# Kernel optimization log

Hardware: AMD Instinct MI355X
Metric: run time of the kernel (lower is better)

## Reference

```python
import jax, jax.numpy as jnp
import numpy as np

HIDDEN = 1024

def setup_inputs() -> dict:
    key = jax.random.key(0)
    ks = jax.random.split(key, 8)
    B, Ti, Tt, V, H, U, K = 4, 2048, 2048, 32000, 1024, 4096, 3
    return {
        "inputs": jax.random.randint(ks[0], (B, Ti), 0, V, dtype=jnp.int32),
        "targets": jax.random.randint(ks[1], (B, Tt), 0, V, dtype=jnp.int32),
        "input_emb": jax.random.normal(ks[2], (V, H), jnp.float32) * 0.02,
        "target_emb": jax.random.normal(ks[3], (V, H), jnp.float32) * 0.02,
        "conv_w": jax.random.normal(ks[4], (K, H, U), jnp.float32) * 0.02,
        "conv_b": jnp.zeros((U,), jnp.float32),
        "dense_w": jax.random.normal(ks[5], (U, H), jnp.float32) * 0.02,
        "dense_b": jnp.zeros((H,), jnp.float32),
    }

def reference(inputs, targets, input_emb, target_emb, conv_w, conv_b, dense_w, dense_b):
    emb_scale = jnp.asarray(HIDDEN, jnp.float32) ** 0.5
    # EmbeddingSharedWeights: gather + sqrt(hidden) scaling
    ie = jnp.take(input_emb, inputs, axis=0) * emb_scale    # [B, Ti, H]
    te = jnp.take(target_emb, targets, axis=0) * emb_scale  # [B, Tt, H]
    # manual scaled dot-product cross-attention (no masks: defaults are None)
    dk = jnp.asarray(ie.shape[-1], jnp.float32)
    logits = jnp.einsum("btd,bsd->bts", te, ie) / jnp.sqrt(dk)  # [B, Tt, Ti]
    weights = jax.nn.softmax(logits, axis=-1)
    attn = jnp.einsum("bts,bsd->btd", weights, ie)              # [B, Tt, H]
    # LanguageModel: Conv1D(units, kernel_size, same) + relu + Dense(hidden)
    h = jax.lax.conv_general_dilated(
        attn, conv_w, window_strides=(1,), padding="SAME",
        dimension_numbers=("NWC", "WIO", "NWC")) + conv_b        # [B, Tt, U]
    h = jax.nn.relu(h)
    out = jnp.einsum("btu,uh->bth", h, dense_w) + dense_b       # [B, Tt, H]
    return out
```

## Files before the change

### kernel.cpp

```cpp
#include <hip/hip_runtime.h>
#include <cstddef>

static constexpr int HID = 1024;
static constexpr int NB  = 4;
static constexpr int TT  = 2048;
static constexpr int UD  = 4096;
static constexpr int PR  = TT + 1;

typedef short bf8    __attribute__((ext_vector_type(8)));
typedef float f32x4  __attribute__((ext_vector_type(4)));

__device__ __forceinline__ unsigned short f2bf(float x) {
  unsigned int u = __float_as_uint(x);
  u += 0x7fffu + ((u >> 16) & 1u);
  return (unsigned short)(u >> 16);
}
__device__ __forceinline__ float bf2f(unsigned short h) {
  return __uint_as_float(((unsigned int)h) << 16);
}
__device__ __forceinline__ unsigned short cvt_bf(float x) { return f2bf(x); }
__device__ __forceinline__ unsigned short cvt_bf(unsigned short x) { return x; }

__device__ __forceinline__ void g2l16(const unsigned short* g, unsigned short* l) {
  __builtin_amdgcn_global_load_lds(
      (const __attribute__((address_space(1))) unsigned int*)g,
      (__attribute__((address_space(3))) unsigned int*)l, 16, 0, 0);
}

#define BARX() __builtin_amdgcn_s_barrier()
#define VMCNT(n) asm volatile("s_waitcnt vmcnt(" #n ")" ::: "memory")

__device__ __forceinline__ void xcd_swz(int& bx, int& by, int& bz) {
  const int gx = gridDim.x, gy = gridDim.y;
  const int nwg = gx * gy * (int)gridDim.z;
  int flat = bx + gx * (by + gy * bz);
  const int cpx = nwg >> 3;
  flat = (flat & 7) * cpx + (flat >> 3);
  bx = flat % gx; flat /= gx;
  by = flat % gy; bz = flat / gy;
}

__global__ __launch_bounds__(256) void gather_split_k(
    const int* __restrict__ idx, const float* __restrict__ emb,
    unsigned short* __restrict__ hi, unsigned short* __restrict__ lo, float scale)
{
  const int row = blockIdx.x;
  const int r = idx[row];
  const int c = threadIdx.x * 4;
  float4 v = *(const float4*)(emb + (size_t)r * HID + c);
  v.x *= scale; v.y *= scale; v.z *= scale; v.w *= scale;
  ushort4 h, l;
  h.x = f2bf(v.x); h.y = f2bf(v.y); h.z = f2bf(v.z); h.w = f2bf(v.w);
  l.x = f2bf(v.x - bf2f(h.x)); l.y = f2bf(v.y - bf2f(h.y));
  l.z = f2bf(v.z - bf2f(h.z)); l.w = f2bf(v.w - bf2f(h.w));
  *(ushort4*)(hi + (size_t)row * HID + c) = h;
  *(ushort4*)(lo + (size_t)row * HID + c) = l;
}

__global__ __launch_bounds__(256) void zero_guard_k(unsigned short* __restrict__ p)
{
  unsigned short* row = p + (size_t)blockIdx.x * PR * HID;
  *(ushort4*)(row + threadIdx.x * 4) = (ushort4){0, 0, 0, 0};
}

template<typename TIN>
__global__ __launch_bounds__(256) void transpose_bf_k(
    const TIN* __restrict__ in, unsigned short* __restrict__ out,
    int R, int C, long long sIn, long long sOut)
{
  __shared__ unsigned short tile[32][33];
  in  += (size_t)blockIdx.z * sIn;
  out += (size_t)blockIdx.z * sOut;
  const int r0 = blockIdx.y * 32, c0 = blockIdx.x * 32;
  const int tc = threadIdx.x & 31, tr8 = threadIdx.x >> 5;
#pragma unroll
  for (int p = 0; p < 4; ++p) {
    const int r = tr8 + p * 8;
    tile[r][tc] = cvt_bf(in[(size_t)(r0 + r) * C + c0 + tc]);
  }
  __syncthreads();
#pragma unroll
  for (int p = 0; p < 4; ++p) {
    const int c = tr8 + p * 8;
    out[(size_t)(c0 + c) * R + r0 + tc] = tile[tc][c];
  }
}

__global__ __launch_bounds__(256) void softmax_bf_k(
    const float* __restrict__ L, unsigned short* __restrict__ W)
{
  const float* row = L + (size_t)blockIdx.x * TT;
  unsigned short* wout = W + (size_t)blockIdx.x * TT;
  const int tid = threadIdx.x;
  float4 v0 = ((const float4*)row)[tid * 2];
  float4 v1 = ((const float4*)row)[tid * 2 + 1];
  float mx = fmaxf(fmaxf(fmaxf(v0.x, v0.y), fmaxf(v0.z, v0.w)),
                   fmaxf(fmaxf(v1.x, v1.y), fmaxf(v1.z, v1.w)));
#pragma unroll
  for (int off = 32; off > 0; off >>= 1)
    mx = fmaxf(mx, __shfl_xor(mx, off, 64));
  __shared__ float sred[8];
  const int wid = tid >> 6;
  if ((tid & 63) == 0) sred[wid] = mx;
  __syncthreads();
  mx = fmaxf(fmaxf(sred[0], sred[1]), fmaxf(sred[2], sred[3]));
  v0.x = __expf(v0.x - mx); v0.y = __expf(v0.y - mx);
  v0.z = __expf(v0.z - mx); v0.w = __expf(v0.w - mx);
  v1.x = __expf(v1.x - mx); v1.y = __expf(v1.y - mx);
  v1.z = __expf(v1.z - mx); v1.w = __expf(v1.w - mx);
  float s = v0.x + v0.y + v0.z + v0.w + v1.x + v1.y + v1.z + v1.w;
#pragma unroll
  for (int off = 32; off > 0; off >>= 1)
    s += __shfl_xor(s, off, 64);
  if ((tid & 63) == 0) sred[4 + wid] = s;
  __syncthreads();
  s = sred[4] + sred[5] + sred[6] + sred[7];
  const float inv = 1.0f / s;
  ushort4 o0, o1;
  o0.x = f2bf(v0.x * inv); o0.y = f2bf(v0.y * inv);
  o0.z = f2bf(v0.z * inv); o0.w = f2bf(v0.w * inv);
  o1.x = f2bf(v1.x * inv); o1.y = f2bf(v1.y * inv);
  o1.z = f2bf(v1.z * inv); o1.w = f2bf(v1.w * inv);
  *(ushort4*)(wout + tid * 8)     = o0;
  *(ushort4*)(wout + tid * 8 + 4) = o1;
}

__device__ __forceinline__ void stage256(
    const unsigned short* __restrict__ P, int ld, int r0, int kk,
    unsigned short* lds, int tid)
{
  const int ke = (((tid & 3) ^ ((tid >> 3) & 3)) << 3);
  const int row = r0 + (tid >> 2);
  g2l16(P + (size_t)row * ld + kk + ke, lds + tid * 8);
  g2l16(P + (size_t)(row + 128) * ld + kk + ke, lds + 4096 + tid * 8);
}
__device__ __forceinline__ void stage128(
    const unsigned short* __restrict__ P, int ld, int r0, int kk,
    unsigned short* lds, int tid)
{
  const int ke = (((tid & 3) ^ ((tid >> 3) & 3)) << 3);
  const int row = r0 + (tid >> 2);
  g2l16(P + (size_t)row * ld + kk + ke, lds + tid * 8);
}

template<int CONVA>
__device__ __forceinline__ void stage_half(
    const unsigned short* __restrict__ P, int ld, int r0, int t, int ks,
    unsigned short* lds, int tid)
{
  const int bk = t * 64 + ks * 32;
  const int ke = (((tid & 3) ^ ((tid >> 3) & 3)) << 3);
  int rowbase, kcol;
  if constexpr (CONVA) {
    const int seg = bk >> 10;
    kcol = (bk & 1023) + ke;
    rowbase = r0 + (tid >> 2) + seg - 1;
  } else {
    kcol = bk + ke;
    rowbase = r0 + (tid >> 2);
  }
#pragma unroll
  for (int c = 0; c < 2; ++c)
    g2l16(P + (ptrdiff_t)(rowbase + c * 128) * ld + kcol,
          lds + c * 4096 + tid * 8);
}

template<int OUTBF, int EPI, int CONVA>
__global__ __launch_bounds__(512, 2) void gemm256_k(
    const unsigned short* __restrict__ A, long long sA, int lda,
    const unsigned short* __restrict__ B, long long sB, int ldb,
    void* __restrict__ Cv, long long sC, int ldc,
    int K, const float* __restrict__ bias)
{
  __shared__ __align__(16) unsigned short As[2][2][256 * 32];
  __shared__ __align__(16) unsigned short Bs[2][2][256 * 32];
  const int tid = threadIdx.x;
  int bxi = blockIdx.x, byi = blockIdx.y, bzi = blockIdx.z;
  xcd_swz(bxi, byi, bzi);
  A += (size_t)bzi * sA;
  B += (size_t)bzi * sB;
  const int bm = byi * 256;
  const int bn = bxi * 256;
  const int wave = tid >> 6, lane = tid & 63;
  const int wr = wave >> 2, wcn = wave & 3;
  const int q = lane >> 4, l16 = lane & 15;
  const int ksw = ((q ^ ((l16 >> 1) & 3)) << 3);
  const int abase = (wr * 128 + l16) * 32 + ksw;
  const int bbase = (wcn * 64 + l16) * 32 + ksw;

  f32x4 acc[8][4];
#pragma unroll
  for (int i = 0; i < 8; ++i)
#pragma unroll
    for (int j = 0; j < 4; ++j)
      acc[i][j] = (f32x4){0.f, 0.f, 0.f, 0.f};

  const int T = K >> 6;

  stage_half<CONVA>(A, lda, bm, 0, 0, &As[0][0][0], tid);
  stage_half<0>   (B, ldb, bn, 0, 0, &Bs[0][0][0], tid);
  stage_half<CONVA>(A, lda, bm, 0, 1, &As[0][1][0], tid);
  stage_half<0>   (B, ldb, bn, 0, 1, &Bs[0][1][0], tid);
  VMCNT(4);
  BARX();

  bf8 af[4], bfr[4];
  for (int t = 0; t < T; ++t) {
    const int buf = t & 1;
    unsigned short* An0 = &As[buf ^ 1][0][0];
    unsigned short* An1 = &As[buf ^ 1][1][0];
    unsigned short* Bn0 = &Bs[buf ^ 1][0][0];
    unsigned short* Bn1 = &Bs[buf ^ 1][1][0];
    const bool next = (t + 1 < T);

#pragma unroll
    for (int j = 0; j < 4; ++j) bfr[j] = *(const bf8*)&Bs[buf][0][bbase + j * 512];
#pragma unroll
    for (int m = 0; m < 4; ++m) af[m] = *(const bf8*)&As[buf][0][abase + m * 512];
    if (next) stage_half<CONVA>(A, lda, bm, t + 1, 0, An0, tid);
    BARX();
    __builtin_amdgcn_s_setprio(1);
#pragma unroll
    for (int m = 0; m < 4; ++m)
#pragma unroll
      for (int j = 0; j < 4; ++j)
        acc[m][j] = __builtin_amdgcn_mfma_f32_16x16x32_bf16(af[m], bfr[j], acc[m][j], 0, 0, 0);
    __builtin_amdgcn_s_setprio(0);
    BARX();

#pragma unroll
    for (int m = 0; m < 4; ++m) af[m] = *(const bf8*)&As[buf][0][abase + (4 + m) * 512];
    if (next) { stage_half<0>(B, ldb, bn, t + 1, 0, Bn0, tid); VMCNT(4); }
    else      { VMCNT(0); }
    BARX();
    __builtin_amdgcn_s_setprio(1);
#pragma unroll
    for (int m = 0; m < 4; ++m)
#pragma unroll
      for (int j = 0; j < 4; ++j)
        acc[4 + m][j] = __builtin_amdgcn_mfma_f32_16x16x32_bf16(af[m], bfr[j], acc[4 + m][j], 0, 0, 0);
    __builtin_amdgcn_s_setprio(0);
    BARX();

#pragma unroll
    for (int j = 0; j < 4; ++j) bfr[j] = *(const bf8*)&Bs[buf][1][bbase + j * 512];
#pragma unroll
    for (int m = 0; m < 4; ++m) af[m] = *(const bf8*)&As[buf][1][abase + m * 512];
    if (next) stage_half<CONVA>(A, lda, bm, t + 1, 1, An1, tid);
    BARX();
    __builtin_amdgcn_s_setprio(1);
#pragma unroll
    for (int m = 0; m < 4; ++m)
#pragma unroll
      for (int j = 0; j < 4; ++j)
        acc[m][j] = __builtin_amdgcn_mfma_f32_16x16x32_bf16(af[m], bfr[j], acc[m][j], 0, 0, 0);
    __builtin_amdgcn_s_setprio(0);
    BARX();

#pragma unroll
    for (int m = 0; m < 4; ++m) af[m] = *(const bf8*)&As[buf][1][abase + (4 + m) * 512];
    if (next) { stage_half<0>(B, ldb, bn, t + 1, 1, Bn1, tid); VMCNT(4); }
    BARX();
    __builtin_amdgcn_s_setprio(1);
#pragma unroll
    for (int m = 0; m < 4; ++m)
#pragma unroll
      for (int j = 0; j < 4; ++j)
        acc[4 + m][j] = __builtin_amdgcn_mfma_f32_16x16x32_bf16(af[m], bfr[j], acc[4 + m][j], 0, 0, 0);
    __builtin_amdgcn_s_setprio(0);
    BARX();
  }

  float* Cf          = (float*)Cv          + (size_t)bzi * sC;
  unsigned short* Cb = (unsigned short*)Cv + (size_t)bzi * sC;
#pragma unroll
  for (int j = 0; j < 4; ++j) {
    const int col = bn + wcn * 64 + j * 16 + l16;
    float bv = 0.f;
    if constexpr (EPI >= 1) bv = bias[col];
#pragma unroll
    for (int i = 0; i < 8; ++i) {
      const int row0 = bm + wr * 128 + i * 16 + q * 4;
#pragma unroll
      for (int r = 0; r < 4; ++r) {
        float v = acc[i][j][r];
        if constexpr (EPI >= 1) v += bv;
        if constexpr (EPI == 2) v = fmaxf(v, 0.f);
        if constexpr (OUTBF) Cb[(size_t)(row0 + r) * ldc + col] = f2bf(v);
        else                 Cf[(size_t)(row0 + r) * ldc + col] = v;
      }
    }
  }
}

template<int OUTBF, int EPI>
__global__ __launch_bounds__(512, 2) void gemm128_k(
    const unsigned short* __restrict__ A, long long sA, int lda,
    const unsigned short* __restrict__ B, long long sB, int ldb,
    void* __restrict__ Cv, long long sC, int ldc,
    int K, const float* __restrict__ bias)
{
  __shared__ __align__(16) unsigned short As[2][2][128 * 32];
  __shared__ __align__(16) unsigned short Bs[2][2][256 * 32];
  const int tid = threadIdx.x;
  int bxi = blockIdx.x, byi = blockIdx.y, bzi = blockIdx.z;
  xcd_swz(bxi, byi, bzi);
  A += (size_t)bzi * sA;
  B += (size_t)bzi * sB;
  const int bm = byi * 128;
  const int bn = bxi * 256;
  const int wave = tid >> 6, lane = tid & 63;
  const int wr = wave >> 2, wcn = wave & 3;
  const int q = lane >> 4, l16 = lane & 15;
  const int ksw = ((q ^ ((l16 >> 1) & 3)) << 3);
  const int abase = (wr * 64 + l16) * 32 + ksw;
  const int bbase = (wcn * 64 + l16) * 32 + ksw;

  f32x4 acc[4][4];
#pragma unroll
  for (int i = 0; i < 4; ++i)
#pragma unroll
    for (int j = 0; j < 4; ++j)
      acc[i][j] = (f32x4){0.f, 0.f, 0.f, 0.f};

  const int T = K >> 6;

  stage128(A, lda, bm, 0,  &As[0][0][0], tid);
  stage256(B, ldb, bn, 0,  &Bs[0][0][0], tid);
  stage128(A, lda, bm, 32, &As[0][1][0], tid);
  stage256(B, ldb, bn, 32, &Bs[0][1][0], tid);
  VMCNT(3);
  BARX();

  bf8 af[4], bfr[4];
  for (int t = 0; t < T; ++t) {
    const int buf = t & 1;
    const bool next = (t + 1 < T);
    const int kk = (t + 1) * 64;

#pragma unroll
    for (int j = 0; j < 4; ++j) bfr[j] = *(const bf8*)&Bs[buf][0][bbase + j * 512];
#pragma unroll
    for (int m = 0; m < 4; ++m) af[m] = *(const bf8*)&As[buf][0][abase + m * 512];
    if (next) {
      stage128(A, lda, bm, kk,      &As[buf ^ 1][0][0], tid);
      stage256(B, ldb, bn, kk,      &Bs[buf ^ 1][0][0], tid);
      VMCNT(3);
    } else { VMCNT(0); }
    BARX();
    __builtin_amdgcn_s_setprio(1);
#pragma unroll
    for (int m = 0; m < 4; ++m)
#pragma unroll
      for (int j = 0; j < 4; ++j)
        acc[m][j] = __builtin_amdgcn_mfma_f32_16x16x32_bf16(af[m], bfr[j], acc[m][j], 0, 0, 0);
    __builtin_amdgcn_s_setprio(0);
    BARX();

#pragma unroll
    for (int j = 0; j < 4; ++j) bfr[j] = *(const bf8*)&Bs[buf][1][bbase + j * 512];
#pragma unroll
    for (int m = 0; m < 4; ++m) af[m] = *(const bf8*)&As[buf][1][abase + m * 512];
    if (next) {
      stage128(A, lda, bm, kk + 32, &As[buf ^ 1][1][0], tid);
      stage256(B, ldb, bn, kk + 32, &Bs[buf ^ 1][1][0], tid);
      VMCNT(3);
    }
    BARX();
    __builtin_amdgcn_s_setprio(1);
#pragma unroll
    for (int m = 0; m < 4; ++m)
#pragma unroll
      for (int j = 0; j < 4; ++j)
        acc[m][j] = __builtin_amdgcn_mfma_f32_16x16x32_bf16(af[m], bfr[j], acc[m][j], 0, 0, 0);
    __builtin_amdgcn_s_setprio(0);
    BARX();
  }

  float* Cf          = (float*)Cv          + (size_t)bzi * sC;
  unsigned short* Cb = (unsigned short*)Cv + (size_t)bzi * sC;
#pragma unroll
  for (int j = 0; j < 4; ++j) {
    const int col = bn + wcn * 64 + j * 16 + l16;
    float bv = 0.f;
    if constexpr (EPI >= 1) bv = bias[col];
#pragma unroll
    for (int i = 0; i < 4; ++i) {
      const int row0 = bm + wr * 64 + i * 16 + q * 4;
#pragma unroll
      for (int r = 0; r < 4; ++r) {
        float v = acc[i][j][r];
        if constexpr (EPI >= 1) v += bv;
        if constexpr (EPI == 2) v = fmaxf(v, 0.f);
        if constexpr (OUTBF) Cb[(size_t)(row0 + r) * ldc + col] = f2bf(v);
        else                 Cf[(size_t)(row0 + r) * ldc + col] = v;
      }
    }
  }
}

__global__ __launch_bounds__(512, 2) void gemm_logits256_k(
    const unsigned short* __restrict__ Ah, const unsigned short* __restrict__ Al,
    const unsigned short* __restrict__ Bh, const unsigned short* __restrict__ Bl,
    float* __restrict__ C)
{
  __shared__ __align__(16) unsigned short AsH[2][256 * 32];
  __shared__ __align__(16) unsigned short AsL[2][256 * 32];
  __shared__ __align__(16) unsigned short BsH[2][256 * 32];
  __shared__ __align__(16) unsigned short BsL[2][256 * 32];
  const int tid = threadIdx.x;
  int bxi = blockIdx.x, byi = blockIdx.y, bzi = blockIdx.z;
  xcd_swz(bxi, byi, bzi);
  const long long SE = (long long)TT * HID;
  Ah += (size_t)bzi * SE; Al += (size_t)bzi * SE;
  Bh += (size_t)bzi * SE; Bl += (size_t)bzi * SE;
  C  += (size_t)bzi * TT * TT;
  const int bm = byi * 256;
  const int bn = bxi * 256;
  const int wave = tid >> 6, lane = tid & 63;
  const int wr = wave >> 2, wcn = wave & 3;
  const int q = lane >> 4, l16 = lane & 15;
  const int ksw = ((q ^ ((l16 >> 1) & 3)) << 3);
  const int abase = (wr * 128 + l16) * 32 + ksw;
  const int bbase = (wcn * 64 + l16) * 32 + ksw;

  f32x4 acc[8][4];
#pragma unroll
  for (int i = 0; i < 8; ++i)
#pragma unroll
    for (int j = 0; j < 4; ++j)
      acc[i][j] = (f32x4){0.f, 0.f, 0.f, 0.f};

  const int T = HID / 32;

  stage256(Ah, HID, bm, 0, &AsH[0][0], tid);
  stage256(Bh, HID, bn, 0, &BsH[0][0], tid);
  stage256(Al, HID, bm, 0, &AsL[0][0], tid);
  stage256(Bl, HID, bn, 0, &BsL[0][0], tid);
  VMCNT(4);
  BARX();

  bf8 bh[4], bl[4], a0[4], a1[4], a2[4], a3[4];
  for (int t = 0; t < T; ++t) {
    const int buf = t & 1;
    const bool next = (t + 1 < T);
    const int kk = (t + 1) * 32;

#pragma unroll
    for (int j = 0; j < 4; ++j) bh[j] = *(const bf8*)&BsH[buf][bbase + j * 512];
#pragma unroll
    for (int m = 0; m < 4; ++m) a0[m] = *(const bf8*)&AsH[buf][abase + m * 512];
    if (next) stage256(Ah, HID, bm, kk, &AsH[buf ^ 1][0], tid);
    BARX();
    __builtin_amdgcn_s_setprio(1);
#pragma unroll
    for (int m = 0; m < 4; ++m)
#pragma unroll
      for (int j = 0; j < 4; ++j)
        acc[m][j] = __builtin_amdgcn_mfma_f32_16x16x32_bf16(a0[m], bh[j], acc[m][j], 0, 0, 0);
    __builtin_amdgcn_s_setprio(0);
    BARX();

#pragma unroll
    for (int m = 0; m < 4; ++m) a1[m] = *(const bf8*)&AsH[buf][abase + (4 + m) * 512];
    if (next) { stage256(Bh, HID, bn, kk, &BsH[buf ^ 1][0], tid); VMCNT(4); }
    else      { VMCNT(0); }
    BARX();
    __builtin_amdgcn_s_setprio(1);
#pragma unroll
    for (int m = 0; m < 4; ++m)
#pragma unroll
      for (int j = 0; j < 4; ++j)
        acc[4 + m][j] = __builtin_amdgcn_mfma_f32_16x16x32_bf16(a1[m], bh[j], acc[4 + m][j], 0, 0, 0);
    __builtin_amdgcn_s_setprio(0);
    BARX();

#pragma unroll
    for (int j = 0; j < 4; ++j) bl[j] = *(const bf8*)&BsL[buf][bbase + j * 512];
#pragma unroll
    for (int m = 0; m < 4; ++m) a2[m] = *(const bf8*)&AsL[buf][abase + m * 512];
    if (next) stage256(Al, HID, bm, kk, &AsL[buf ^ 1][0], tid);
    BARX();
    __builtin_amdgcn_s_setprio(1);
#pragma unroll
    for (int m = 0; m < 4; ++m)
#pragma unroll
      for (int j = 0; j < 4; ++j) {
        acc[m][j] = __builtin_amdgcn_mfma_f32_16x16x32_bf16(a0[m], bl[j], acc[m][j], 0, 0, 0);
        acc[m][j] = __builtin_amdgcn_mfma_f32_16x16x32_bf16(a2[m], bh[j], acc[m][j], 0, 0, 0);
      }
    __builtin_amdgcn_s_setprio(0);
    BARX();

#pragma unroll
    for (int m = 0; m < 4; ++m) a3[m] = *(const bf8*)&AsL[buf][abase + (4 + m) * 512];
    if (next) { stage256(Bl, HID, bn, kk, &BsL[buf ^ 1][0], tid); VMCNT(4); }
    BARX();
    __builtin_amdgcn_s_setprio(1);
#pragma unroll
    for (int m = 0; m < 4; ++m)
#pragma unroll
      for (int j = 0; j < 4; ++j) {
        acc[4 + m][j] = __builtin_amdgcn_mfma_f32_16x16x32_bf16(a1[m], bl[j], acc[4 + m][j], 0, 0, 0);
        acc[4 + m][j] = __builtin_amdgcn_mfma_f32_16x16x32_bf16(a3[m], bh[j], acc[4 + m][j], 0, 0, 0);
      }
    __builtin_amdgcn_s_setprio(0);
    BARX();
  }

#pragma unroll
  for (int j = 0; j < 4; ++j) {
    const int col = bn + wcn * 64 + j * 16 + l16;
#pragma unroll
    for (int i = 0; i < 8; ++i) {
      const int row0 = bm + wr * 128 + i * 16 + q * 4;
#pragma unroll
      for (int r = 0; r < 4; ++r)
        C[(size_t)(row0 + r) * TT + col] = acc[i][j][r];
    }
  }
}

extern "C" void kernel_launch(void* const* d_in, const int* in_sizes, int n_in,
                              void* d_out, int out_size, void* d_ws, size_t ws_size,
                              hipStream_t stream)
{
  const int*   inputs     = (const int*)d_in[0];
  const int*   targets    = (const int*)d_in[1];
  const float* input_emb  = (const float*)d_in[2];
  const float* target_emb = (const float*)d_in[3];
  const float* conv_w     = (const float*)d_in[4];
  const float* conv_b     = (const float*)d_in[5];
  const float* dense_w    = (const float*)d_in[6];
  const float* dense_b    = (const float*)d_in[7];
  float* out = (float*)d_out;

  const long long SE = (long long)TT * HID;
  const size_t SZ = (size_t)NB * SE * 2;

  char* base = (char*)d_ws;
  unsigned short* te_hi = (unsigned short*)(base);
  unsigned short* te_lo = (unsigned short*)(base + SZ);
  unsigned short* ie_hi = (unsigned short*)(base + 2 * SZ);
  unsigned short* ie_lo = (unsigned short*)(base + 3 * SZ);
  float*          logit = (float*)         (base + 4 * SZ);
  unsigned short* Wbf   = (unsigned short*)(base + 4 * SZ + (size_t)NB * TT * TT * 4);
  unsigned short* ieT     = (unsigned short*)(base);
  unsigned short* attnP   = (unsigned short*)(base + SZ);
  unsigned short* attnD   = attnP + (size_t)HID;
  unsigned short* convwb  = (unsigned short*)(base + 2 * SZ + 16384);
  unsigned short* hb      = (unsigned short*)(base + 4 * SZ);
  unsigned short* densewb = (unsigned short*)Wbf;

  gather_split_k<<<NB * TT, 256, 0, stream>>>(targets, target_emb, te_hi, te_lo, 1.0f);
  gather_split_k<<<NB * TT, 256, 0, stream>>>(inputs,  input_emb,  ie_hi, ie_lo, 32.0f);

  gemm_logits256_k<<<dim3(TT / 256, TT / 256, NB), 512, 0, stream>>>(
      te_hi, te_lo, ie_hi, ie_lo, logit);

  transpose_bf_k<unsigned short><<<dim3(HID / 32, TT / 32, NB), 256, 0, stream>>>(
      ie_hi, ieT, TT, HID, SE, SE);

  softmax_bf_k<<<NB * TT, 256, 0, stream>>>(logit, Wbf);

  zero_guard_k<<<NB + 1, 256, 0, stream>>>(attnP);
  gemm128_k<1, 0><<<dim3(HID / 256, TT / 128, NB), 512, 0, stream>>>(
      Wbf, (long long)TT * TT, TT, ieT, SE, TT,
      attnD, (long long)PR * HID, HID, TT, nullptr);

  transpose_bf_k<float><<<dim3(UD / 32, (3 * HID) / 32, 1), 256, 0, stream>>>(
      conv_w, convwb, 3 * HID, UD, 0, 0);
  transpose_bf_k<float><<<dim3(HID / 32, UD / 32, 1), 256, 0, stream>>>(
      dense_w, densewb, UD, HID, 0, 0);

  gemm256_k<1, 2, 1><<<dim3(UD / 256, TT / 256, NB), 512, 0, stream>>>(
      attnD, (long long)PR * HID, HID, convwb, 0, 3 * HID,
      hb, (long long)TT * UD, UD, 3 * HID, conv_b);

  gemm128_k<0, 1><<<dim3(HID / 256, TT / 128, NB), 512, 0, stream>>>(
      hb, (long long)TT * UD, UD, densewb, 0, UD,
      out, SE, HID, UD, dense_b);
}
```

Measured before the change: 724.5 us.

## Deepen global-to-LDS prefetch to three half-tiles in flight across GEMM kernels

Reorders staging in three bf16 MFMA GEMM kernels so that each half-tile load is issued as soon as its LDS slot is free, keeping about one and a half K-steps of loads in flight instead of one. The prologue stages an extra half-tile, and the vmcnt waits are raised to match. The aim is to hide more global memory latency behind MFMA work. The cost is more outstanding loads per wave, and buffer-reuse hazards that depend on exact barrier placement.

Result: no change. 724.5 us (-0.0%).

```diff
diff --git a/kernel.cpp b/kernel.cpp
--- a/kernel.cpp
+++ b/kernel.cpp
@@ -201,23 +201,20 @@
   stage_half<0>   (B, ldb, bn, 0, 0, &Bs[0][0][0], tid);
   stage_half<CONVA>(A, lda, bm, 0, 1, &As[0][1][0], tid);
   stage_half<0>   (B, ldb, bn, 0, 1, &Bs[0][1][0], tid);
-  VMCNT(4);
+  stage_half<CONVA>(A, lda, bm, 1, 0, &As[1][0][0], tid);
+  stage_half<0>   (B, ldb, bn, 1, 0, &Bs[1][0][0], tid);
+  VMCNT(8);
   BARX();
 
   bf8 af[4], bfr[4];
   for (int t = 0; t < T; ++t) {
     const int buf = t & 1;
-    unsigned short* An0 = &As[buf ^ 1][0][0];
-    unsigned short* An1 = &As[buf ^ 1][1][0];
-    unsigned short* Bn0 = &Bs[buf ^ 1][0][0];
-    unsigned short* Bn1 = &Bs[buf ^ 1][1][0];
-    const bool next = (t + 1 < T);
 
 #pragma unroll
     for (int j = 0; j < 4; ++j) bfr[j] = *(const bf8*)&Bs[buf][0][bbase + j * 512];
 #pragma unroll
     for (int m = 0; m < 4; ++m) af[m] = *(const bf8*)&As[buf][0][abase + m * 512];
-    if (next) stage_half<CONVA>(A, lda, bm, t + 1, 0, An0, tid);
+    if (t + 1 < T) stage_half<CONVA>(A, lda, bm, t + 1, 1, &As[buf ^ 1][1][0], tid);
     BARX();
     __builtin_amdgcn_s_setprio(1);
 #pragma unroll
@@ -230,8 +227,8 @@
 
 #pragma unroll
     for (int m = 0; m < 4; ++m) af[m] = *(const bf8*)&As[buf][0][abase + (4 + m) * 512];
-    if (next) { stage_half<0>(B, ldb, bn, t + 1, 0, Bn0, tid); VMCNT(4); }
-    else      { VMCNT(0); }
+    if (t + 1 < T) stage_half<0>(B, ldb, bn, t + 1, 1, &Bs[buf ^ 1][1][0], tid);
+    if (t < T - 1) { VMCNT(8); } else { VMCNT(0); }
     BARX();
     __builtin_amdgcn_s_setprio(1);
 #pragma unroll
@@ -246,7 +243,7 @@
     for (int j = 0; j < 4; ++j) bfr[j] = *(const bf8*)&Bs[buf][1][bbase + j * 512];
 #pragma unroll
     for (int m = 0; m < 4; ++m) af[m] = *(const bf8*)&As[buf][1][abase + m * 512];
-    if (next) stage_half<CONVA>(A, lda, bm, t + 1, 1, An1, tid);
+    if (t + 2 < T) stage_half<CONVA>(A, lda, bm, t + 2, 0, &As[buf][0][0], tid);
     BARX();
     __builtin_amdgcn_s_setprio(1);
 #pragma unroll
@@ -259,7 +256,8 @@
 
 #pragma unroll
     for (int m = 0; m < 4; ++m) af[m] = *(const bf8*)&As[buf][1][abase + (4 + m) * 512];
-    if (next) { stage_half<0>(B, ldb, bn, t + 1, 1, Bn1, tid); VMCNT(4); }
+    if (t + 2 < T) stage_half<0>(B, ldb, bn, t + 2, 0, &Bs[buf][0][0], tid);
+    if (t < T - 2) { VMCNT(8); } else { VMCNT(0); }
     BARX();
     __builtin_amdgcn_s_setprio(1);
 #pragma unroll
@@ -329,24 +327,25 @@
   stage256(B, ldb, bn, 0,  &Bs[0][0][0], tid);
   stage128(A, lda, bm, 32, &As[0][1][0], tid);
   stage256(B, ldb, bn, 32, &Bs[0][1][0], tid);
-  VMCNT(3);
+  stage128(A, lda, bm, 64, &As[1][0][0], tid);
+  stage256(B, ldb, bn, 64, &Bs[1][0][0], tid);
+  VMCNT(6);
   BARX();
 
   bf8 af[4], bfr[4];
   for (int t = 0; t < T; ++t) {
     const int buf = t & 1;
-    const bool next = (t + 1 < T);
-    const int kk = (t + 1) * 64;
 
 #pragma unroll
     for (int j = 0; j < 4; ++j) bfr[j] = *(const bf8*)&Bs[buf][0][bbase + j * 512];
 #pragma unroll
     for (int m = 0; m < 4; ++m) af[m] = *(const bf8*)&As[buf][0][abase + m * 512];
-    if (next) {
-      stage128(A, lda, bm, kk,      &As[buf ^ 1][0][0], tid);
-      stage256(B, ldb, bn, kk,      &Bs[buf ^ 1][0][0], tid);
-      VMCNT(3);
-    } else { VMCNT(0); }
+    if (t + 1 < T) {
+      const int kk = (t + 1) * 64 + 32;
+      stage128(A, lda, bm, kk, &As[buf ^ 1][1][0], tid);
+      stage256(B, ldb, bn, kk, &Bs[buf ^ 1][1][0], tid);
+    }
+    if (t < T - 1) { VMCNT(6); } else { VMCNT(0); }
     BARX();
     __builtin_amdgcn_s_setprio(1);
 #pragma unroll
@@ -361,11 +360,12 @@
     for (int j = 0; j < 4; ++j) bfr[j] = *(const bf8*)&Bs[buf][1][bbase + j * 512];
 #pragma unroll
     for (int m = 0; m < 4; ++m) af[m] = *(const bf8*)&As[buf][1][abase + m * 512];
-    if (next) {
-      stage128(A, lda, bm, kk + 32, &As[buf ^ 1][1][0], tid);
-      stage256(B, ldb, bn, kk + 32, &Bs[buf ^ 1][1][0], tid);
-      VMCNT(3);
+    if (t + 2 < T) {
+      const int kk = (t + 2) * 64;
+      stage128(A, lda, bm, kk, &As[buf][0][0], tid);
+      stage256(B, ldb, bn, kk, &Bs[buf][0][0], tid);
     }
+    if (t < T - 2) { VMCNT(6); } else { VMCNT(0); }
     BARX();
     __builtin_amdgcn_s_setprio(1);
 #pragma unroll
@@ -433,24 +433,24 @@
 
   const int T = HID / 32;
 
-  stage256(Ah, HID, bm, 0, &AsH[0][0], tid);
-  stage256(Bh, HID, bn, 0, &BsH[0][0], tid);
-  stage256(Al, HID, bm, 0, &AsL[0][0], tid);
-  stage256(Bl, HID, bn, 0, &BsL[0][0], tid);
-  VMCNT(4);
+  stage256(Ah, HID, bm, 0,  &AsH[0][0], tid);
+  stage256(Bh, HID, bn, 0,  &BsH[0][0], tid);
+  stage256(Al, HID, bm, 0,  &AsL[0][0], tid);
+  stage256(Bl, HID, bn, 0,  &BsL[0][0], tid);
+  stage256(Ah, HID, bm, 32, &AsH[1][0], tid);
+  stage256(Bh, HID, bn, 32, &BsH[1][0], tid);
+  VMCNT(8);
   BARX();
 
   bf8 bh[4], bl[4], a0[4], a1[4], a2[4], a3[4];
   for (int t = 0; t < T; ++t) {
     const int buf = t & 1;
-    const bool next = (t + 1 < T);
-    const int kk = (t + 1) * 32;
 
 #pragma unroll
     for (int j = 0; j < 4; ++j) bh[j] = *(const bf8*)&BsH[buf][bbase + j * 512];
 #pragma unroll
     for (int m = 0; m < 4; ++m) a0[m] = *(const bf8*)&AsH[buf][abase + m * 512];
-    if (next) stage256(Ah, HID, bm, kk, &AsH[buf ^ 1][0], tid);
+    if (t + 1 < T) stage256(Al, HID, bm, (t + 1) * 32, &AsL[buf ^ 1][0], tid);
     BARX();
     __builtin_amdgcn_s_setprio(1);
 #pragma unroll
@@ -463,8 +463,8 @@
 
 #pragma unroll
     for (int m = 0; m < 4; ++m) a1[m] = *(const bf8*)&AsH[buf][abase + (4 + m) * 512];
-    if (next) { stage256(Bh, HID, bn, kk, &BsH[buf ^ 1][0], tid); VMCNT(4); }
-    else      { VMCNT(0); }
+    if (t + 1 < T) stage256(Bl, HID, bn, (t + 1) * 32, &BsL[buf ^ 1][0], tid);
+    if (t < T - 1) { VMCNT(8); } else { VMCNT(0); }
     BARX();
     __builtin_amdgcn_s_setprio(1);
 #pragma unroll
@@ -479,7 +479,7 @@
     for (int j = 0; j < 4; ++j) bl[j] = *(const bf8*)&BsL[buf][bbase + j * 512];
 #pragma unroll
     for (int m = 0; m < 4; ++m) a2[m] = *(const bf8*)&AsL[buf][abase + m * 512];
-    if (next) stage256(Al, HID, bm, kk, &AsL[buf ^ 1][0], tid);
+    if (t + 2 < T) stage256(Ah, HID, bm, (t + 2) * 32, &AsH[buf][0], tid);
     BARX();
     __builtin_amdgcn_s_setprio(1);
 #pragma unroll
@@ -494,7 +494,8 @@
 
 #pragma unroll
     for (int m = 0; m < 4; ++m) a3[m] = *(const bf8*)&AsL[buf][abase + (4 + m) * 512];
-    if (next) { stage256(Bl, HID, bn, kk, &BsL[buf ^ 1][0], tid); VMCNT(4); }
+    if (t + 2 < T) stage256(Bh, HID, bn, (t + 2) * 32, &BsH[buf][0], tid);
+    if (t < T - 2) { VMCNT(8); } else { VMCNT(0); }
     BARX();
     __builtin_amdgcn_s_setprio(1);
 #pragma unroll
```
